# Kernel tuning notes

Measured on AMD Instinct MI355X. Metric: run time of the kernel, lower is better.

The kernel has to match this reference:

```python
import jax, jax.numpy as jnp
import numpy as np

BIOSYNTHETIC_FAMILIES = {'glutamate': ['E','Q','P','R','K'], 'aspartate': ['D','N','T','I','M','K'], 'serine': ['S','G','C'], 'pyruvate': ['A','V','L'], 'aromatic': ['F','Y','W'], 'histidine': ['H']}
CODON_TABLE = {'UUU':'F','UUC':'F','UUA':'L','UUG':'L','CUU':'L','CUC':'L','CUA':'L','CUG':'L','AUU':'I','AUC':'I','AUA':'I','AUG':'M','GUU':'V','GUC':'V','GUA':'V','GUG':'V','UCU':'S','UCC':'S','UCA':'S','UCG':'S','CCU':'P','CCC':'P','CCA':'P','CCG':'P','ACU':'T','ACC':'T','ACA':'T','ACG':'T','GCU':'A','GCC':'A','GCA':'A','GCG':'A','UAU':'Y','UAC':'Y','UAA':'*','UAG':'*','CAU':'H','CAC':'H','CAA':'Q','CAG':'Q','AAU':'N','AAC':'N','AAA':'K','AAG':'K','GAU':'D','GAC':'D','GAA':'E','GAG':'E','UGU':'C','UGC':'C','UGA':'*','UGG':'W','CGU':'R','CGC':'R','CGA':'R','CGG':'R','AGU':'S','AGC':'S','AGA':'R','AGG':'R','GGU':'G','GGC':'G','GGA':'G','GGG':'G'}

def _build_family_matrix():
    aa2fam = {aa: f for f, aas in BIOSYNTHETIC_FAMILIES.items() for aa in aas}
    codons = list(CODON_TABLE.keys())
    fam = [aa2fam.get(CODON_TABLE[c]) for c in codons]  # None for stop codons
    M = np.zeros((64, 64), dtype=np.float32)
    for i in range(64):
        for j in range(64):
            if fam[i] is not None and fam[j] is not None and fam[i] == fam[j]:
                M[i, j] = 1.0
    return jnp.asarray(M)

FAMILY_MATRIX = _build_family_matrix()  # (64, 64) constant lookup table

def setup_inputs() -> dict:
    key = jax.random.key(0)
    k1, k2 = jax.random.split(key)
    codon_embeddings = jax.random.normal(k1, (16, 512, 16), dtype=jnp.float32)
    codon_indices = jax.random.randint(k2, (16, 512), 0, 64, dtype=jnp.int64 if jax.config.jax_enable_x64 else jnp.int32)
    return {"codon_embeddings": codon_embeddings, "codon_indices": codon_indices}

def reference(codon_embeddings, codon_indices):
    b, s, d = codon_embeddings.shape
    emb = codon_embeddings.reshape(-1, d)            # (n, d)
    idx = codon_indices.reshape(-1)                  # (n,)
    # Euclidean pairwise distances (torch.cdist, p=2)
    sq = jnp.sum(emb * emb, axis=-1)                 # (n,)
    d2 = sq[:, None] + sq[None, :] - 2.0 * (emb @ emb.T)
    d2 = jnp.maximum(d2, 0.0)
    mask = d2 > 0.0
    dist = jnp.where(mask, jnp.sqrt(jnp.where(mask, d2, 1.0)), 0.0)  # (n, n)
    # Same-family mask via 64x64 lookup gather
    same = FAMILY_MATRIX[idx[:, None], idx[None, :]]  # (n, n)
    eps = 1e-10
    same_sum = jnp.sum(same)
    total = jnp.asarray(dist.shape[0] * dist.shape[1], dist.dtype)
    same_d = jnp.sum(dist * same) / (same_sum + eps)
    diff_d = (jnp.sum(dist) - jnp.sum(dist * same)) / ((total - same_sum) + eps)
    loss = same_d - 0.5 * diff_d + 1.0
    return jax.nn.relu(loss)
```

## Files before the change

### kernel.cpp

```cpp
#include <hip/hip_runtime.h>
#include <math.h>

#define N_ROWS 8192
#define D 16
#define TILE 128
#define NT 64
#define NBLK 2080

#define OFF_PT   0
#define OFF_PS   16384

typedef short  bf16x8 __attribute__((ext_vector_type(8)));
typedef float  f32x4  __attribute__((ext_vector_type(4)));

#define BF_ONE ((unsigned short)0x3F80)

__device__ __constant__ signed char FAM_LUT[64] = {
  4,4,3,3, 3,3,3,3,
  1,1,1,1, 3,3,3,3,
  2,2,2,2, 0,0,0,0,
  1,1,1,1, 3,3,3,3,
  4,4,-1,-1, 5,5,0,0,
  1,1,1,1, 1,1,0,0,
  2,2,-1,4, 0,0,0,0,
  2,2,0,0, 2,2,2,2
};

__device__ __forceinline__ unsigned short f2bf(float f) {
  unsigned u = __float_as_uint(f);
  u += 0x7fffu + ((u >> 16) & 1u);
  return (unsigned short)(u >> 16);
}
__device__ __forceinline__ float bf2f(unsigned short s) {
  return __uint_as_float((unsigned)s << 16);
}
__device__ __forceinline__ float sqrt_abs(float x) {
  const float ax = __builtin_fabsf(x);
  float r;
  asm("v_sqrt_f32 %0, %1" : "=v"(r) : "v"(ax));
  return r;
}

__global__ __launch_bounds__(512, 4) void pair_kernel(
    const float* __restrict__ emb, const int* __restrict__ idx,
    float* __restrict__ pt, float* __restrict__ ps) {
  const int u = blockIdx.y, bx = blockIdx.x;
  int it, jt;
  if (bx < NT - u) { it = u;          jt = u + bx; }
  else             { it = NT - 1 - u; jt = bx - 1; }

  __shared__ __align__(16) unsigned short LB1[4096];
  __shared__ __align__(16) unsigned short LFB[1024];
  __shared__ __align__(16) unsigned short LFA[1024];
  __shared__ float SQIF[TILE];
  __shared__ float rT[8], rS[8];

  const int t  = threadIdx.x;
  const int w  = t >> 6;
  const int l  = t & 63;
  const int lr = l & 15;
  const int g  = l >> 4;

  if (t < 256) {
    const int  local = t & 127;
    const bool iside = (t < 128);
    const int  row = (iside ? it : jt) * TILE + local;
    const float4* s4 = (const float4*)(emb + (size_t)row * D);
    float4 a0 = s4[0], a1 = s4[1], a2 = s4[2], a3 = s4[3];
    float v[16];
    v[0]=a0.x; v[1]=a0.y; v[2]=a0.z; v[3]=a0.w;
    v[4]=a1.x; v[5]=a1.y; v[6]=a1.z; v[7]=a1.w;
    v[8]=a2.x; v[9]=a2.y; v[10]=a2.z; v[11]=a2.w;
    v[12]=a3.x; v[13]=a3.y; v[14]=a3.z; v[15]=a3.w;
    unsigned short bh[16];
#pragma unroll
    for (int k = 0; k < 16; ++k) bh[k] = f2bf(v[k]);
    float ss = bf2f(bh[0]) * bf2f(bh[0]);
#pragma unroll
    for (int k = 1; k < 16; ++k) { const float rv = bf2f(bh[k]); ss = fmaf(rv, rv, ss); }
    const int f = FAM_LUT[idx[row] & 63];
    unsigned short oh[8];
#pragma unroll
    for (int k = 0; k < 8; ++k) oh[k] = (f == k) ? BF_ONE : (unsigned short)0;
    if (iside) {
      SQIF[local] = ss;
      *(bf16x8*)(LFA + local * 8) = *(bf16x8*)oh;
    } else {
      const unsigned short sqh = f2bf(ss);
      const unsigned short sql = f2bf(ss - bf2f(sqh));
      unsigned short c2[8] = {sqh, sql, BF_ONE, BF_ONE, 0, 0, 0, 0};
      unsigned short cz[8] = {0, 0, 0, 0, 0, 0, 0, 0};
      unsigned short* d1 = LB1 + local * 32;
      *(bf16x8*)(d1 + 0)  = *(bf16x8*)&bh[0];
      *(bf16x8*)(d1 + 8)  = *(bf16x8*)&bh[8];
      *(bf16x8*)(d1 + 16) = *(bf16x8*)c2;
      *(bf16x8*)(d1 + 24) = *(bf16x8*)cz;
      *(bf16x8*)(LFB + local * 8) = *(bf16x8*)oh;
    }
  }

  const int arow = it * TILE + w * 16 + lr;
  const float4* a4 = (const float4*)(emb + (size_t)arow * D + (g & 1) * 8);
  float4 c0 = a4[0], c1 = a4[1];
  float va[8];
  va[0]=c0.x; va[1]=c0.y; va[2]=c0.z; va[3]=c0.w;
  va[4]=c1.x; va[5]=c1.y; va[6]=c1.z; va[7]=c1.w;
  unsigned short f8[8];
#pragma unroll
  for (int k = 0; k < 8; ++k) f8[k] = f2bf(-2.0f * va[k]);

  __syncthreads();

  if (g >= 2) {
#pragma unroll
    for (int k = 0; k < 8; ++k) f8[k] = 0;
    if (g == 2) {
      const float sq = SQIF[w * 16 + lr];
      const unsigned short sqh = f2bf(sq);
      f8[0] = BF_ONE; f8[1] = BF_ONE;
      f8[2] = sqh;    f8[3] = f2bf(sq - bf2f(sqh));
    }
  }
  const bf16x8 afrag = *(bf16x8*)f8;
  bf16x8 afrag3;
  if (g == 0) afrag3 = *(const bf16x8*)(LFA + (w * 16 + lr) * 8);
  else        { bf16x8 z = {0,0,0,0,0,0,0,0}; afrag3 = z; }

  bf16x8 b1f[8], m3[8];
#pragma unroll
  for (int mj = 0; mj < 8; ++mj)
    b1f[mj] = *(const bf16x8*)(LB1 + (mj * 16 + lr) * 32 + g * 8);
  if (g == 0) {
#pragma unroll
    for (int mj = 0; mj < 8; ++mj)
      m3[mj] = *(const bf16x8*)(LFB + (mj * 16 + lr) * 8);
  } else {
    bf16x8 z = {0,0,0,0,0,0,0,0};
#pragma unroll
    for (int mj = 0; mj < 8; ++mj) m3[mj] = z;
  }

  const f32x4 zf = {0.0f, 0.0f, 0.0f, 0.0f};
  float accT = 0.0f, accS = 0.0f;
#pragma unroll
  for (int mj = 0; mj < 8; ++mj) {
    const f32x4 acc = __builtin_amdgcn_mfma_f32_16x16x32_bf16(afrag,  b1f[mj], zf, 0, 0, 0);
    const f32x4 msk = __builtin_amdgcn_mfma_f32_16x16x32_bf16(afrag3, m3[mj],  zf, 0, 0, 0);
#pragma unroll
    for (int r = 0; r < 4; ++r) {
      const float dist = sqrt_abs(acc[r]);
      accT += dist;
      accS = fmaf(msk[r], dist, accS);
    }
  }

#pragma unroll
  for (int off = 32; off > 0; off >>= 1) {
    accT += __shfl_down(accT, off);
    accS += __shfl_down(accS, off);
  }
  if (l == 0) { rT[w] = accT; rS[w] = accS; }
  __syncthreads();
  if (t == 0) {
    float sT = 0.0f, sS = 0.0f;
#pragma unroll
    for (int k = 0; k < 8; ++k) { sT += rT[k]; sS += rS[k]; }
    const float wgt = (it == jt) ? 1.0f : 2.0f;
    const int bid = blockIdx.y * gridDim.x + blockIdx.x;
    pt[bid] = wgt * sT;
    ps[bid] = wgt * sS;
  }
}

__global__ __launch_bounds__(1024) void final_kernel(
    const float* __restrict__ pt, const float* __restrict__ ps,
    const int* __restrict__ idx, float* __restrict__ out) {
  const int t = threadIdx.x, w = t >> 6, l = t & 63;
  __shared__ float  HW[16][8];
  __shared__ double rTd[16], rSd[16];

  const int4* p4 = (const int4*)idx;
  const int4 va = p4[t], vb = p4[t + 1024];
  int vals[8] = {va.x, va.y, va.z, va.w, vb.x, vb.y, vb.z, vb.w};
  float myCnt = 0.0f;
#pragma unroll
  for (int rr = 0; rr < 8; ++rr) {
    const int f = FAM_LUT[vals[rr] & 63];
#pragma unroll
    for (int fam = 0; fam < 6; ++fam) {
      const unsigned long long mk = __ballot(f == fam);
      if (l == fam) myCnt += (float)__popcll(mk);
    }
  }
  if (l < 8) HW[w][l] = (l < 6) ? myCnt : 0.0f;

  double sT = 0.0, sS = 0.0;
  for (int k = t; k < NBLK; k += 1024) { sT += (double)pt[k]; sS += (double)ps[k]; }
#pragma unroll
  for (int off = 32; off > 0; off >>= 1) {
    sT += __shfl_down(sT, off);
    sS += __shfl_down(sS, off);
  }
  if (l == 0) { rTd[w] = sT; rSd[w] = sS; }
  __syncthreads();
  if (t == 0) {
    double tot = 0.0, sam = 0.0;
#pragma unroll
    for (int k = 0; k < 16; ++k) { tot += rTd[k]; sam += rSd[k]; }
    double same_sum = 0.0;
    for (int f = 0; f < 6; ++f) {
      double c = 0.0;
      for (int k = 0; k < 16; ++k) c += (double)HW[k][f];
      same_sum += c * c;
    }
    const double total  = (double)N_ROWS * (double)N_ROWS;
    const double same_d = sam / (same_sum + 1e-10);
    const double diff_d = (tot - sam) / (total - same_sum + 1e-10);
    double loss = same_d - 0.5 * diff_d + 1.0;
    out[0] = (float)(loss > 0.0 ? loss : 0.0);
  }
}

extern "C" void kernel_launch(void* const* d_in, const int* in_sizes, int n_in,
                              void* d_out, int out_size, void* d_ws, size_t ws_size,
                              hipStream_t stream) {
  const float* emb = (const float*)d_in[0];
  const int*   idx = (const int*)d_in[1];
  char* ws = (char*)d_ws;
  float* pt = (float*)(ws + OFF_PT);
  float* ps = (float*)(ws + OFF_PS);

  pair_kernel<<<dim3(NT + 1, NT / 2), dim3(512), 0, stream>>>(emb, idx, pt, ps);
  final_kernel<<<dim3(1), dim3(1024), 0, stream>>>(pt, ps, idx, (float*)d_out);
}
```

Baseline: 23.64 us.

## Precompute packed bf16 operand rows in a prep kernel before pair kernel

Adds a prep kernel that converts each embedding row once into padded bf16 A and B MFMA operand rows (including squared-norm hi/lo terms) plus a one-hot family vector, all stored in workspace. The pair kernel then copies these prepacked rows straight into LDS and registers, instead of redoing the bf16 conversion, norm computation and LUT lookup in each of the 2080 tiles. This removes redundant per-tile conversion work and one LDS stage, but adds a third kernel launch and extra global traffic for the packed buffers. The A operand is now -2 times the bf16-rounded value rather than the fp32 value, which slightly changes rounding.

```diff
diff --git a/kernel.cpp b/kernel.cpp
--- a/kernel.cpp
+++ b/kernel.cpp
@@ -9,6 +9,9 @@
 
 #define OFF_PT   0
 #define OFF_PS   16384
+#define OFF_AP   32768
+#define OFF_BP   557056
+#define OFF_FOH  1081344
 
 typedef short  bf16x8 __attribute__((ext_vector_type(8)));
 typedef float  f32x4  __attribute__((ext_vector_type(4)));
@@ -41,8 +44,54 @@
   return r;
 }
 
+__global__ __launch_bounds__(256) void prep_kernel(
+    const float* __restrict__ emb, const int* __restrict__ idx,
+    unsigned short* __restrict__ aP, unsigned short* __restrict__ bP,
+    unsigned short* __restrict__ foh) {
+  const int i = blockIdx.x * 256 + threadIdx.x;
+  const float4* s4 = (const float4*)(emb + (size_t)i * D);
+  float4 a0 = s4[0], a1 = s4[1], a2 = s4[2], a3 = s4[3];
+  float v[16];
+  v[0]=a0.x; v[1]=a0.y; v[2]=a0.z; v[3]=a0.w;
+  v[4]=a1.x; v[5]=a1.y; v[6]=a1.z; v[7]=a1.w;
+  v[8]=a2.x; v[9]=a2.y; v[10]=a2.z; v[11]=a2.w;
+  v[12]=a3.x; v[13]=a3.y; v[14]=a3.z; v[15]=a3.w;
+
+  unsigned short bh[16];
+#pragma unroll
+  for (int k = 0; k < 16; ++k) bh[k] = f2bf(v[k]);
+  float ss = bf2f(bh[0]) * bf2f(bh[0]);
+#pragma unroll
+  for (int k = 1; k < 16; ++k) { const float rv = bf2f(bh[k]); ss = fmaf(rv, rv, ss); }
+  const unsigned short sqh = f2bf(ss);
+  const unsigned short sql = f2bf(ss - bf2f(sqh));
+
+  unsigned short A[32], B[32];
+#pragma unroll
+  for (int k = 0; k < 16; ++k) {
+    A[k] = f2bf(-2.0f * bf2f(bh[k]));
+    B[k] = bh[k];
+  }
+  A[16] = BF_ONE; A[17] = BF_ONE; A[18] = sqh; A[19] = sql;
+  B[16] = sqh;    B[17] = sql;    B[18] = BF_ONE; B[19] = BF_ONE;
+#pragma unroll
+  for (int k = 20; k < 32; ++k) { A[k] = 0; B[k] = 0; }
+
+#pragma unroll
+  for (int c = 0; c < 4; ++c) {
+    *(bf16x8*)(aP + (size_t)i * 32 + c * 8) = *(bf16x8*)&A[c * 8];
+    *(bf16x8*)(bP + (size_t)i * 32 + c * 8) = *(bf16x8*)&B[c * 8];
+  }
+  const int f = FAM_LUT[idx[i] & 63];
+  unsigned short oh[8];
+#pragma unroll
+  for (int k = 0; k < 8; ++k) oh[k] = (f == k) ? BF_ONE : (unsigned short)0;
+  *(bf16x8*)(foh + (size_t)i * 8) = *(bf16x8*)oh;
+}
+
 __global__ __launch_bounds__(512, 4) void pair_kernel(
-    const float* __restrict__ emb, const int* __restrict__ idx,
+    const unsigned short* __restrict__ aP, const unsigned short* __restrict__ bP,
+    const unsigned short* __restrict__ foh,
     float* __restrict__ pt, float* __restrict__ ps) {
   const int u = blockIdx.y, bx = blockIdx.x;
   int it, jt;
@@ -51,8 +100,6 @@
 
   __shared__ __align__(16) unsigned short LB1[4096];
   __shared__ __align__(16) unsigned short LFB[1024];
-  __shared__ __align__(16) unsigned short LFA[1024];
-  __shared__ float SQIF[TILE];
   __shared__ float rT[8], rS[8];
 
   const int t  = threadIdx.x;
@@ -61,70 +108,17 @@
   const int lr = l & 15;
   const int g  = l >> 4;
 
-  if (t < 256) {
-    const int  local = t & 127;
-    const bool iside = (t < 128);
-    const int  row = (iside ? it : jt) * TILE + local;
-    const float4* s4 = (const float4*)(emb + (size_t)row * D);
-    float4 a0 = s4[0], a1 = s4[1], a2 = s4[2], a3 = s4[3];
-    float v[16];
-    v[0]=a0.x; v[1]=a0.y; v[2]=a0.z; v[3]=a0.w;
-    v[4]=a1.x; v[5]=a1.y; v[6]=a1.z; v[7]=a1.w;
-    v[8]=a2.x; v[9]=a2.y; v[10]=a2.z; v[11]=a2.w;
-    v[12]=a3.x; v[13]=a3.y; v[14]=a3.z; v[15]=a3.w;
-    unsigned short bh[16];
-#pragma unroll
-    for (int k = 0; k < 16; ++k) bh[k] = f2bf(v[k]);
-    float ss = bf2f(bh[0]) * bf2f(bh[0]);
-#pragma unroll
-    for (int k = 1; k < 16; ++k) { const float rv = bf2f(bh[k]); ss = fmaf(rv, rv, ss); }
-    const int f = FAM_LUT[idx[row] & 63];
-    unsigned short oh[8];
-#pragma unroll
-    for (int k = 0; k < 8; ++k) oh[k] = (f == k) ? BF_ONE : (unsigned short)0;
-    if (iside) {
-      SQIF[local] = ss;
-      *(bf16x8*)(LFA + local * 8) = *(bf16x8*)oh;
-    } else {
-      const unsigned short sqh = f2bf(ss);
-      const unsigned short sql = f2bf(ss - bf2f(sqh));
-      unsigned short c2[8] = {sqh, sql, BF_ONE, BF_ONE, 0, 0, 0, 0};
-      unsigned short cz[8] = {0, 0, 0, 0, 0, 0, 0, 0};
-      unsigned short* d1 = LB1 + local * 32;
-      *(bf16x8*)(d1 + 0)  = *(bf16x8*)&bh[0];
-      *(bf16x8*)(d1 + 8)  = *(bf16x8*)&bh[8];
-      *(bf16x8*)(d1 + 16) = *(bf16x8*)c2;
-      *(bf16x8*)(d1 + 24) = *(bf16x8*)cz;
-      *(bf16x8*)(LFB + local * 8) = *(bf16x8*)oh;
-    }
-  }
+  *(bf16x8*)(LB1 + t * 8) = *(const bf16x8*)(bP + (size_t)jt * 4096 + t * 8);
+  if (t < TILE)
+    *(bf16x8*)(LFB + t * 8) = *(const bf16x8*)(foh + (size_t)jt * 1024 + t * 8);
 
   const int arow = it * TILE + w * 16 + lr;
-  const float4* a4 = (const float4*)(emb + (size_t)arow * D + (g & 1) * 8);
-  float4 c0 = a4[0], c1 = a4[1];
-  float va[8];
-  va[0]=c0.x; va[1]=c0.y; va[2]=c0.z; va[3]=c0.w;
-  va[4]=c1.x; va[5]=c1.y; va[6]=c1.z; va[7]=c1.w;
-  unsigned short f8[8];
-#pragma unroll
-  for (int k = 0; k < 8; ++k) f8[k] = f2bf(-2.0f * va[k]);
+  const bf16x8 afrag = *(const bf16x8*)(aP + (size_t)arow * 32 + g * 8);
+  bf16x8 afrag3;
+  if (g == 0) afrag3 = *(const bf16x8*)(foh + (size_t)arow * 8);
+  else        { bf16x8 z = {0,0,0,0,0,0,0,0}; afrag3 = z; }
 
   __syncthreads();
-
-  if (g >= 2) {
-#pragma unroll
-    for (int k = 0; k < 8; ++k) f8[k] = 0;
-    if (g == 2) {
-      const float sq = SQIF[w * 16 + lr];
-      const unsigned short sqh = f2bf(sq);
-      f8[0] = BF_ONE; f8[1] = BF_ONE;
-      f8[2] = sqh;    f8[3] = f2bf(sq - bf2f(sqh));
-    }
-  }
-  const bf16x8 afrag = *(bf16x8*)f8;
-  bf16x8 afrag3;
-  if (g == 0) afrag3 = *(const bf16x8*)(LFA + (w * 16 + lr) * 8);
-  else        { bf16x8 z = {0,0,0,0,0,0,0,0}; afrag3 = z; }
 
   bf16x8 b1f[8], m3[8];
 #pragma unroll
@@ -227,9 +221,13 @@
   const float* emb = (const float*)d_in[0];
   const int*   idx = (const int*)d_in[1];
   char* ws = (char*)d_ws;
-  float* pt = (float*)(ws + OFF_PT);
-  float* ps = (float*)(ws + OFF_PS);
-
-  pair_kernel<<<dim3(NT + 1, NT / 2), dim3(512), 0, stream>>>(emb, idx, pt, ps);
+  float*          pt  = (float*)(ws + OFF_PT);
+  float*          ps  = (float*)(ws + OFF_PS);
+  unsigned short* aP  = (unsigned short*)(ws + OFF_AP);
+  unsigned short* bP  = (unsigned short*)(ws + OFF_BP);
+  unsigned short* foh = (unsigned short*)(ws + OFF_FOH);
+
+  prep_kernel<<<dim3(N_ROWS / 256), dim3(256), 0, stream>>>(emb, idx, aP, bP, foh);
+  pair_kernel<<<dim3(NT + 1, NT / 2), dim3(512), 0, stream>>>(aP, bP, foh, pt, ps);
   final_kernel<<<dim3(1), dim3(1024), 0, stream>>>(pt, ps, idx, (float*)d_out);
 }
```

After: 26.20 us. 1.11x slower.

## Process two column tiles per block with triangular index decode

Applied to the files above, without the earlier changes.

Each block now computes one row tile against two adjacent column tiles (128x256), so the grid drops from 2080 to 1056 blocks. Block coordinates come from a closed-form triangular decode with sqrt and a fix-up loop, and an out-of-range second tile is zeroed and weighted to zero. B fragments are loaded from LDS inside the MFMA loop rather than preloaded, and sqrt uses the abs source modifier. The aim is to amortize A-tile loading and per-block launch and reduction overhead, at the cost of more LDS per block and some wasted work on edge blocks.

```diff
diff --git a/kernel.cpp b/kernel.cpp
--- a/kernel.cpp
+++ b/kernel.cpp
@@ -5,10 +5,10 @@
 #define D 16
 #define TILE 128
 #define NT 64
-#define NBLK 2080
+#define NPAIR 1056
 
 #define OFF_PT   0
-#define OFF_PS   16384
+#define OFF_PS   8192
 
 typedef short  bf16x8 __attribute__((ext_vector_type(8)));
 typedef float  f32x4  __attribute__((ext_vector_type(4)));
@@ -35,23 +35,34 @@
   return __uint_as_float((unsigned)s << 16);
 }
 __device__ __forceinline__ float sqrt_abs(float x) {
-  const float ax = __builtin_fabsf(x);
   float r;
-  asm("v_sqrt_f32 %0, %1" : "=v"(r) : "v"(ax));
+  asm("v_sqrt_f32 %0, abs(%1)" : "=v"(r) : "v"(x));
   return r;
+}
+__device__ __forceinline__ int S_of(int m) {
+  return (m & 1) ? (((m + 1) * (m + 1)) >> 2) : ((m * (m + 2)) >> 2);
 }
 
 __global__ __launch_bounds__(512, 4) void pair_kernel(
     const float* __restrict__ emb, const int* __restrict__ idx,
     float* __restrict__ pt, float* __restrict__ ps) {
-  const int u = blockIdx.y, bx = blockIdx.x;
-  int it, jt;
-  if (bx < NT - u) { it = u;          jt = u + bx; }
-  else             { it = NT - 1 - u; jt = bx - 1; }
-
-  __shared__ __align__(16) unsigned short LB1[4096];
-  __shared__ __align__(16) unsigned short LFB[1024];
+  const int b = blockIdx.x;
+  const int cc = NPAIR - b;
+  int m = (int)(2.0f * sqrtf((float)cc));
+  if (m > NT) m = NT;
+  if (m < 1) m = 1;
+  while (S_of(m) < cc) ++m;
+  while (m > 1 && S_of(m - 1) >= cc) --m;
+  const int it  = NT - m;
+  const int p   = b - (NPAIR - S_of(m));
+  const int jt0 = it + 2 * p;
+  const int jt1 = jt0 + 1;
+  const bool v1 = (jt1 < NT);
+
+  __shared__ __align__(16) unsigned short LB1[8192];
+  __shared__ __align__(16) unsigned short LFB[2048];
   __shared__ __align__(16) unsigned short LFA[1024];
+  __shared__ __align__(16) unsigned short LZ[8];
   __shared__ float SQIF[TILE];
   __shared__ float rT[8], rS[8];
 
@@ -62,9 +73,11 @@
   const int g  = l >> 4;
 
   if (t < 256) {
-    const int  local = t & 127;
-    const bool iside = (t < 128);
-    const int  row = (iside ? it : jt) * TILE + local;
+    const int  jd    = t >> 7;
+    const int  rl    = t & 127;
+    const int  jtile = jd ? jt1 : jt0;
+    const bool valid = (jtile < NT);
+    const int  row   = min(jtile, NT - 1) * TILE + rl;
     const float4* s4 = (const float4*)(emb + (size_t)row * D);
     float4 a0 = s4[0], a1 = s4[1], a2 = s4[2], a3 = s4[3];
     float v[16];
@@ -74,29 +87,47 @@
     v[12]=a3.x; v[13]=a3.y; v[14]=a3.z; v[15]=a3.w;
     unsigned short bh[16];
 #pragma unroll
-    for (int k = 0; k < 16; ++k) bh[k] = f2bf(v[k]);
+    for (int k = 0; k < 16; ++k) bh[k] = valid ? f2bf(v[k]) : (unsigned short)0;
     float ss = bf2f(bh[0]) * bf2f(bh[0]);
 #pragma unroll
     for (int k = 1; k < 16; ++k) { const float rv = bf2f(bh[k]); ss = fmaf(rv, rv, ss); }
+    const unsigned short sqh = f2bf(ss);
+    const unsigned short sql = f2bf(ss - bf2f(sqh));
+    unsigned short c2[8] = {sqh, sql, BF_ONE, BF_ONE, 0, 0, 0, 0};
+    if (!valid) { c2[0] = 0; c2[1] = 0; c2[2] = 0; c2[3] = 0; }
+    unsigned short cz[8] = {0, 0, 0, 0, 0, 0, 0, 0};
+    unsigned short* d1 = LB1 + t * 32;
+    *(bf16x8*)(d1 + 0)  = *(bf16x8*)&bh[0];
+    *(bf16x8*)(d1 + 8)  = *(bf16x8*)&bh[8];
+    *(bf16x8*)(d1 + 16) = *(bf16x8*)c2;
+    *(bf16x8*)(d1 + 24) = *(bf16x8*)cz;
+    const int f = valid ? FAM_LUT[idx[row] & 63] : -9;
+    unsigned short oh[8];
+#pragma unroll
+    for (int k = 0; k < 8; ++k) oh[k] = (f == k) ? BF_ONE : (unsigned short)0;
+    *(bf16x8*)(LFB + t * 8) = *(bf16x8*)oh;
+  } else if (t < 384) {
+    const int local = t - 256;
+    const int row = it * TILE + local;
+    const float4* s4 = (const float4*)(emb + (size_t)row * D);
+    float4 a0 = s4[0], a1 = s4[1], a2 = s4[2], a3 = s4[3];
+    float v[16];
+    v[0]=a0.x; v[1]=a0.y; v[2]=a0.z; v[3]=a0.w;
+    v[4]=a1.x; v[5]=a1.y; v[6]=a1.z; v[7]=a1.w;
+    v[8]=a2.x; v[9]=a2.y; v[10]=a2.z; v[11]=a2.w;
+    v[12]=a3.x; v[13]=a3.y; v[14]=a3.z; v[15]=a3.w;
+    float ss = 0.0f;
+#pragma unroll
+    for (int k = 0; k < 16; ++k) { const float rv = bf2f(f2bf(v[k])); ss = fmaf(rv, rv, ss); }
+    SQIF[local] = ss;
     const int f = FAM_LUT[idx[row] & 63];
     unsigned short oh[8];
 #pragma unroll
     for (int k = 0; k < 8; ++k) oh[k] = (f == k) ? BF_ONE : (unsigned short)0;
-    if (iside) {
-      SQIF[local] = ss;
-      *(bf16x8*)(LFA + local * 8) = *(bf16x8*)oh;
-    } else {
-      const unsigned short sqh = f2bf(ss);
-      const unsigned short sql = f2bf(ss - bf2f(sqh));
-      unsigned short c2[8] = {sqh, sql, BF_ONE, BF_ONE, 0, 0, 0, 0};
-      unsigned short cz[8] = {0, 0, 0, 0, 0, 0, 0, 0};
-      unsigned short* d1 = LB1 + local * 32;
-      *(bf16x8*)(d1 + 0)  = *(bf16x8*)&bh[0];
-      *(bf16x8*)(d1 + 8)  = *(bf16x8*)&bh[8];
-      *(bf16x8*)(d1 + 16) = *(bf16x8*)c2;
-      *(bf16x8*)(d1 + 24) = *(bf16x8*)cz;
-      *(bf16x8*)(LFB + local * 8) = *(bf16x8*)oh;
-    }
+    *(bf16x8*)(LFA + local * 8) = *(bf16x8*)oh;
+  } else if (t == 384) {
+    bf16x8 z = {0,0,0,0,0,0,0,0};
+    *(bf16x8*)LZ = z;
   }
 
   const int arow = it * TILE + w * 16 + lr;
@@ -107,7 +138,7 @@
   va[4]=c1.x; va[5]=c1.y; va[6]=c1.z; va[7]=c1.w;
   unsigned short f8[8];
 #pragma unroll
-  for (int k = 0; k < 8; ++k) f8[k] = f2bf(-2.0f * va[k]);
+  for (int k = 0; k < 8; ++k) f8[k] = f2bf(-2.0f * bf2f(f2bf(va[k])));
 
   __syncthreads();
 
@@ -126,34 +157,29 @@
   if (g == 0) afrag3 = *(const bf16x8*)(LFA + (w * 16 + lr) * 8);
   else        { bf16x8 z = {0,0,0,0,0,0,0,0}; afrag3 = z; }
 
-  bf16x8 b1f[8], m3[8];
-#pragma unroll
-  for (int mj = 0; mj < 8; ++mj)
-    b1f[mj] = *(const bf16x8*)(LB1 + (mj * 16 + lr) * 32 + g * 8);
-  if (g == 0) {
-#pragma unroll
-    for (int mj = 0; mj < 8; ++mj)
-      m3[mj] = *(const bf16x8*)(LFB + (mj * 16 + lr) * 8);
-  } else {
-    bf16x8 z = {0,0,0,0,0,0,0,0};
-#pragma unroll
-    for (int mj = 0; mj < 8; ++mj) m3[mj] = z;
-  }
-
+  const unsigned short* p3 = (g == 0) ? (LFB + lr * 8) : LZ;
+  const int step3 = (g == 0) ? 128 : 0;
+  const int boff  = lr * 32 + g * 8;
   const f32x4 zf = {0.0f, 0.0f, 0.0f, 0.0f};
-  float accT = 0.0f, accS = 0.0f;
-#pragma unroll
-  for (int mj = 0; mj < 8; ++mj) {
-    const f32x4 acc = __builtin_amdgcn_mfma_f32_16x16x32_bf16(afrag,  b1f[mj], zf, 0, 0, 0);
-    const f32x4 msk = __builtin_amdgcn_mfma_f32_16x16x32_bf16(afrag3, m3[mj],  zf, 0, 0, 0);
+  float tT0 = 0.0f, tS0 = 0.0f, tT1 = 0.0f, tS1 = 0.0f;
+#pragma unroll
+  for (int mj = 0; mj < 16; ++mj) {
+    const bf16x8 b1f = *(const bf16x8*)(LB1 + (mj * 16) * 32 + boff);
+    const bf16x8 m3  = *(const bf16x8*)(p3 + mj * step3);
+    const f32x4 acc = __builtin_amdgcn_mfma_f32_16x16x32_bf16(afrag,  b1f, zf, 0, 0, 0);
+    const f32x4 msk = __builtin_amdgcn_mfma_f32_16x16x32_bf16(afrag3, m3,  zf, 0, 0, 0);
 #pragma unroll
     for (int r = 0; r < 4; ++r) {
       const float dist = sqrt_abs(acc[r]);
-      accT += dist;
-      accS = fmaf(msk[r], dist, accS);
-    }
-  }
-
+      if (mj < 8) { tT0 += dist; tS0 = fmaf(msk[r], dist, tS0); }
+      else        { tT1 += dist; tS1 = fmaf(msk[r], dist, tS1); }
+    }
+  }
+
+  const float w0 = (jt0 == it) ? 1.0f : 2.0f;
+  const float w1 = v1 ? 2.0f : 0.0f;
+  float accT = fmaf(w0, tT0, w1 * tT1);
+  float accS = fmaf(w0, tS0, w1 * tS1);
 #pragma unroll
   for (int off = 32; off > 0; off >>= 1) {
     accT += __shfl_down(accT, off);
@@ -165,10 +191,8 @@
     float sT = 0.0f, sS = 0.0f;
 #pragma unroll
     for (int k = 0; k < 8; ++k) { sT += rT[k]; sS += rS[k]; }
-    const float wgt = (it == jt) ? 1.0f : 2.0f;
-    const int bid = blockIdx.y * gridDim.x + blockIdx.x;
-    pt[bid] = wgt * sT;
-    ps[bid] = wgt * sS;
+    pt[b] = sT;
+    ps[b] = sS;
   }
 }
 
@@ -195,7 +219,7 @@
   if (l < 8) HW[w][l] = (l < 6) ? myCnt : 0.0f;
 
   double sT = 0.0, sS = 0.0;
-  for (int k = t; k < NBLK; k += 1024) { sT += (double)pt[k]; sS += (double)ps[k]; }
+  for (int k = t; k < NPAIR; k += 1024) { sT += (double)pt[k]; sS += (double)ps[k]; }
 #pragma unroll
   for (int off = 32; off > 0; off >>= 1) {
     sT += __shfl_down(sT, off);
@@ -230,6 +254,6 @@
   float* pt = (float*)(ws + OFF_PT);
   float* ps = (float*)(ws + OFF_PS);
 
-  pair_kernel<<<dim3(NT + 1, NT / 2), dim3(512), 0, stream>>>(emb, idx, pt, ps);
+  pair_kernel<<<dim3(NPAIR), dim3(512), 0, stream>>>(emb, idx, pt, ps);
   final_kernel<<<dim3(1), dim3(1024), 0, stream>>>(pt, ps, idx, (float*)d_out);
 }
```

Result: faster. 21.93 us (-7.2%).
